# Kernel tuning notes

Measured on AMD Instinct MI355X. Metric: run time of the kernel, lower is better.

## Reference

```python
import jax, jax.numpy as jnp
import numpy as np

B, T, D = 2, 2048, 2048
N, K, H = 16, 8, 128  # num_heads, num_kv_heads, head_dim
SOFTCAP = 50.0
ROPE_BASE = 10000.0


def apply_rope(x, positions):
    # x: [B, L, heads, H], positions: [B, L]
    head_dim = x.shape[-1]
    fraction = 2.0 * jnp.arange(head_dim // 2, dtype=jnp.float32) / head_dim
    timescale = ROPE_BASE ** fraction  # [H/2]
    sinusoid = positions.astype(jnp.float32)[..., None] / timescale  # [B, L, H/2]
    sinusoid = sinusoid[..., None, :]  # [B, L, 1, H/2]
    sin, cos = jnp.sin(sinusoid), jnp.cos(sinusoid)
    first, second = jnp.split(x, 2, axis=-1)
    out = jnp.concatenate([first * cos - second * sin,
                           second * cos + first * sin], axis=-1)
    return out.astype(x.dtype)


def setup_inputs() -> dict:
    key = jax.random.key(0)
    kx, kq, kkv, ko = jax.random.split(key, 4)
    x = jax.random.normal(kx, (B, T, D), dtype=jnp.float32)
    positions = jnp.broadcast_to(jnp.arange(T, dtype=jnp.int32), (B, T))
    attn_mask = jnp.broadcast_to(
        jnp.tril(jnp.ones((T, T), dtype=bool))[None, None], (B, 1, T, T))
    # variance-scaling fan_in init approximated with scaled normals
    w_q = jax.random.normal(kq, (N, D, H), dtype=jnp.float32) / np.sqrt(D)
    w_kv = jax.random.normal(kkv, (2, K, D, H), dtype=jnp.float32) / np.sqrt(D)
    w_out = jax.random.normal(ko, (N, H, D), dtype=jnp.float32) / np.sqrt(N * H)
    return {"x": x, "positions": positions, "attn_mask": attn_mask,
            "w_q": w_q, "w_kv": w_kv, "w_out": w_out}


def reference(x, positions, attn_mask, w_q, w_kv, w_out):
    # QKV projections (GQA: separate q and kv einsums)
    q = jnp.einsum('BTD,NDH->BTNH', x, w_q)        # [B,T,N,H]
    kv = jnp.einsum('BSD,cKDH->cBSKH', x, w_kv)     # [2,B,S,K,H]
    k, v = kv[0], kv[1]
    q = apply_rope(q, positions) * (H ** -0.5)      # rsqrt_head_dim norm
    k = apply_rope(k, positions)
    # GQA grouping: N = K * G
    G = N // K
    qg = q.reshape(B, T, K, G, H)
    logits = jnp.einsum('BTKGH,BSKH->BKGTS', qg, k).astype(jnp.float32)
    logits = jnp.tanh(logits / SOFTCAP) * SOFTCAP   # logits softcap
    big_neg = -2.3819763e+38
    masked = jnp.where(attn_mask[:, :, None, :, :], logits, big_neg)
    probs = jax.nn.softmax(masked, axis=-1).astype(k.dtype)
    encoded = jnp.einsum('BKGTS,BSKH->BTKGH', probs, v).reshape(B, T, N, H)
    return jnp.einsum('BTNH,NHD->BTD', encoded, w_out)
```

## Files before the change

### kernel.cpp

```cpp
#include <hip/hip_runtime.h>
#include <math.h>
#include <stdint.h>


typedef unsigned short u16;
using bf16x8 = __attribute__((ext_vector_type(8))) short;
using f32x4  = __attribute__((ext_vector_type(4))) float;

#define MFMA_BF16(a,b,c) __builtin_amdgcn_mfma_f32_16x16x32_bf16((a),(b),(c),0,0,0)

static __device__ __forceinline__ float b2f(u16 u) {
  union { unsigned int i; float f; } v; v.i = ((unsigned int)u) << 16; return v.f;
}
static __device__ __forceinline__ u16 f2b(float f) {
  union { float f; unsigned int i; } v; v.f = f;
  unsigned int r = v.i + 0x7fffu + ((v.i >> 16) & 1u);
  return (u16)(r >> 16);
}
static __device__ __forceinline__ unsigned pk2(float x0, float x1) {
  union { float f; unsigned u; } a, b;
  a.f = x0; b.f = x1;
  return __builtin_amdgcn_perm(b.u + 0x8000u, a.u + 0x8000u, 0x07060302u);
}
static __device__ __forceinline__ void gload_lds16(const void* g, void* l) {
  __builtin_amdgcn_global_load_lds((__attribute__((address_space(1))) void*)(g),
                                   (__attribute__((address_space(3))) void*)(l),
                                   16, 0, 0);
}

__global__ __launch_bounds__(256) void prep(const float* __restrict__ x, u16* __restrict__ xb,
                                            const float* __restrict__ wq,
                                            const float* __restrict__ wkv,
                                            const float* __restrict__ wout,
                                            u16* __restrict__ wqkvt, u16* __restrict__ woutt) {
  const int tid = threadIdx.x;
  int bid = blockIdx.x;
  if (bid < 8192) {
    const int i = (bid * 256 + tid) * 4;
    const float4 v = *(const float4*)(x + i);
    ushort4 o;
    o.x = f2b(v.x); o.y = f2b(v.y); o.z = f2b(v.z); o.w = f2b(v.w);
    *(ushort4*)(xb + i) = o;
    return;
  }
  bid -= 8192;
  const float* src;
  u16* dst;
  int rows, cols, bx, by;
  if (bid < 8192) {
    const int seg = bid >> 12;
    const int r = bid & 4095;
    const int mat = r >> 8;
    bx = (r & 255) & 3;
    by = (r & 255) >> 2;
    rows = 2048; cols = 128;
    src = (seg ? wkv : wq) + (size_t)mat * 2048 * 128;
    dst = wqkvt + (size_t)(seg * 16 + mat) * 2048 * 128;
  } else {
    const int r = bid - 8192;
    bx = r & 63;
    by = r >> 6;
    rows = 2048; cols = 2048;
    src = wout;
    dst = woutt;
  }
  __shared__ u16 tile[32][33];
  const int c0 = bx * 32, r0 = by * 32;
  const int tx = tid & 31, ty = tid >> 5;
#pragma unroll
  for (int j = 0; j < 4; ++j)
    tile[ty + j * 8][tx] = f2b(src[(size_t)(r0 + ty + j * 8) * cols + (c0 + tx)]);
  __syncthreads();
#pragma unroll
  for (int j = 0; j < 4; ++j)
    dst[(size_t)(c0 + ty + j * 8) * rows + (r0 + tx)] = tile[tx][ty + j * 8];
}

__global__ __launch_bounds__(256) void gemm_qkv(const u16* __restrict__ X,
                                                const u16* __restrict__ wqkvt,
                                                u16* __restrict__ qb,
                                                u16* __restrict__ kb,
                                                u16* __restrict__ vtb) {
  __shared__ __align__(16) u16 sA[128 * 64];
  __shared__ __align__(16) u16 sB[128 * 64];
  const int m0 = blockIdx.x * 128;
  const int ct = blockIdx.y;
  const u16* Bt = wqkvt + (size_t)ct * 128 * 2048;
  const int tid = threadIdx.x;
  const int wave = tid >> 6, lane = tid & 63;
  const int wm = wave & 1, wn = wave >> 1;
  const int quad = lane >> 4, l16 = lane & 15;
  const int srow = lane >> 3;
  const int sch = (lane & 7) ^ srow;

  f32x4 acc[4][4] = {};

  for (int k0 = 0; k0 < 2048; k0 += 64) {
#pragma unroll
    for (int s = 0; s < 4; ++s) {
      const int instr = wave * 4 + s;
      const int row = instr * 8 + srow;
      gload_lds16(X + (size_t)(m0 + row) * 2048 + k0 + sch * 8, (char*)sA + instr * 1024);
      gload_lds16(Bt + (size_t)row * 2048 + k0 + sch * 8, (char*)sB + instr * 1024);
    }
    __syncthreads();
#pragma unroll
    for (int ks = 0; ks < 2; ++ks) {
      bf16x8 af[4], bfr[4];
#pragma unroll
      for (int mf = 0; mf < 4; ++mf) {
        const int R = wm * 64 + mf * 16 + l16;
        af[mf] = *(const bf16x8*)((char*)sA + R * 128 + (((ks * 4 + quad) ^ (R & 7)) << 4));
      }
#pragma unroll
      for (int nf = 0; nf < 4; ++nf) {
        const int R = wn * 64 + nf * 16 + l16;
        bfr[nf] = *(const bf16x8*)((char*)sB + R * 128 + (((ks * 4 + quad) ^ (R & 7)) << 4));
      }
#pragma unroll
      for (int mf = 0; mf < 4; ++mf)
#pragma unroll
        for (int nf = 0; nf < 4; ++nf)
          acc[mf][nf] = MFMA_BF16(af[mf], bfr[nf], acc[mf][nf]);
    }
    __syncthreads();
  }

#pragma unroll
  for (int mf = 0; mf < 4; ++mf) {
    const int mm = m0 + wm * 64 + mf * 16 + quad * 4;
    const int b = mm >> 11;
    const int t = mm & 2047;
#pragma unroll
    for (int nf = 0; nf < 4; ++nf) {
      const int h = wn * 64 + nf * 16 + l16;
      if (ct < 16) {
        u16* d = qb + (((size_t)b * 16 + ct) * 2048 + t) * 128 + h;
#pragma unroll
        for (int i = 0; i < 4; ++i) d[(size_t)i * 128] = f2b(acc[mf][nf][i]);
      } else if (ct < 24) {
        u16* d = kb + (((size_t)b * 8 + (ct - 16)) * 2048 + t) * 128 + h;
#pragma unroll
        for (int i = 0; i < 4; ++i) d[(size_t)i * 128] = f2b(acc[mf][nf][i]);
      } else {
        u16* d = vtb + (((size_t)b * 8 + (ct - 24)) * 128 + h) * 2048 + t;
        uint2 pkv;
        pkv.x = (unsigned)f2b(acc[mf][nf][0]) | ((unsigned)f2b(acc[mf][nf][1]) << 16);
        pkv.y = (unsigned)f2b(acc[mf][nf][2]) | ((unsigned)f2b(acc[mf][nf][3]) << 16);
        *(uint2*)d = pkv;
      }
    }
  }
}

__global__ __launch_bounds__(256) void rope_kernel(u16* __restrict__ qb,
                                                   u16* __restrict__ kb,
                                                   const int* __restrict__ pos) {
  const unsigned idx = blockIdx.x * 256 + threadIdx.x;
  const unsigned QP = 1u << 21;
  u16* p;
  float scale;
  int b, t, j2;
  if (idx < QP) {
    j2 = (int)(idx & 31) * 2; t = (int)((idx >> 5) & 2047);
    const int hd = (int)((idx >> 16) & 15); b = (int)(idx >> 20);
    p = qb + (((size_t)b * 16 + hd) * 2048 + t) * 128;
    scale = 0.08838834764831845f;
  } else {
    const unsigned r = idx - QP;
    j2 = (int)(r & 31) * 2; t = (int)((r >> 5) & 2047);
    const int hd = (int)((r >> 16) & 7); b = (int)(r >> 19);
    p = kb + (((size_t)b * 8 + hd) * 2048 + t) * 128;
    scale = 1.0f;
  }
  const float fpos = (float)pos[(size_t)b * 2048 + t];
  const unsigned lo = *(const unsigned*)(p + j2);
  const unsigned hi = *(const unsigned*)(p + j2 + 64);
  unsigned olo = 0, ohi = 0;
#pragma unroll
  for (int d = 0; d < 2; ++d) {
    const int j = j2 + d;
    const float ts = __powf(10000.0f, (float)j * (1.0f / 64.0f));
    float sn, cs;
    sincosf(fpos / ts, &sn, &cs);
    const float a = b2f((u16)((d ? (lo >> 16) : lo) & 0xffffu));
    const float c2 = b2f((u16)((d ? (hi >> 16) : hi) & 0xffffu));
    olo |= ((unsigned)f2b((a * cs - c2 * sn) * scale)) << (16 * d);
    ohi |= ((unsigned)f2b((c2 * cs + a * sn) * scale)) << (16 * d);
  }
  *(unsigned*)(p + j2) = olo;
  *(unsigned*)(p + j2 + 64) = ohi;
}

__global__ __launch_bounds__(256) void attn_fused(const u16* __restrict__ qg,
                                                  const u16* __restrict__ kg,
                                                  const u16* __restrict__ vtg,
                                                  u16* __restrict__ enc) {
  __shared__ __align__(16) char lds[32768];
  char* sK = lds;
  char* sV = lds + 16384;

  const int bid = blockIdx.x;
  const int x = bid & 7;
  const int i6 = bid >> 3;
  const int p = i6 & 15;
  const int head = (i6 >> 4) * 8 + x;
  const int b = head >> 4;
  const int n = head & 15;
  const int kh = n >> 1;

  const u16* qbase = qg + ((size_t)b * 16 + n) * 2048 * 128;
  const u16* kbase = kg + ((size_t)b * 8 + kh) * 2048 * 128;
  const u16* vbase = vtg + ((size_t)b * 8 + kh) * 128 * 2048;

  const int tid = threadIdx.x, wave = tid >> 6, lane = tid & 63;
  const int quad = lane >> 4, l16 = lane & 15;
  const int bp_a0 = ((quad & 1) * 32 + l16) * 4;
  const int bp_a1 = bp_a0 + 64;

  const float L2E = 1.4426950408889634f;
  const float C50 = 72.13475204444817f;
  const float A1 = 1.3333333333e-4f;
  const float A2 = 2.1333333333e-8f;
  const float A3 = 3.4539682540e-12f;

#pragma unroll 1
  for (int pass = 0; pass < 2; ++pass) {
    const int Q = pass ? (31 - p) : p;
    const int tw = Q * 64 + wave * 16;
    const int tlane = tw + l16;

    bf16x8 qf[4];
#pragma unroll
    for (int kf = 0; kf < 4; ++kf)
      qf[kf] = *(const bf16x8*)(qbase + (size_t)tlane * 128 + kf * 32 + quad * 8);

    f32x4 o[8] = {};
    f32x4 lacc = {0.f, 0.f, 0.f, 0.f};

#pragma unroll 1
    for (int si = 0; si <= Q; ++si) {
      const int s0 = si * 64;
      __syncthreads();
#pragma unroll
      for (int r2 = 0; r2 < 4; ++r2) {
        const int idx = r2 * 256 + tid;
        const int kr = idx >> 4, kc = idx & 15;
        *(float4*)(sK + kr * 256 + ((kc ^ (kr & 15)) << 4)) =
            *(const float4*)(kbase + (size_t)(s0 + kr) * 128 + kc * 8);
        const int vr = idx >> 3, vc = idx & 7;
        *(float4*)(sV + vr * 128 + ((vc ^ (vr & 7)) << 4)) =
            *(const float4*)(vbase + (size_t)vr * 2048 + s0 + vc * 8);
      }
      __syncthreads();

      const bool diag = (si == Q);
      const int nfmax = diag ? wave : 3;
      const int kmax = diag ? (wave >> 1) : 1;

      f32x4 sacc[4];
#pragma unroll
      for (int nf = 0; nf < 4; ++nf) {
        if (nf <= nfmax) {
          const int sr = nf * 16 + l16;
          f32x4 a = {0.f, 0.f, 0.f, 0.f};
#pragma unroll
          for (int kf = 0; kf < 4; ++kf) {
            const bf16x8 kfr =
                *(const bf16x8*)(sK + sr * 256 + (((kf * 4 + quad) ^ (sr & 15)) << 4));
            a = MFMA_BF16(kfr, qf[kf], a);
          }
          sacc[nf] = a;
        }
      }

#pragma unroll
      for (int nf = 0; nf < 4; ++nf) {
        if (nf <= nfmax) {
          const f32x4 xv = sacc[nf];
          const f32x4 u = xv * xv;
          f32x4 t = u * (-A3) + A2;
          t = u * t + (-A1);
          t = u * t + 1.0f;
          const f32x4 tc = xv * t;
          f32x4 pv;
#pragma unroll
          for (int i = 0; i < 4; ++i) pv[i] = exp2f(fmaf(tc[i], L2E, -C50));
          if (diag) {
#pragma unroll
            for (int i = 0; i < 4; ++i) {
              const int sg = s0 + nf * 16 + quad * 4 + i;
              if (sg > tlane) pv[i] = 0.0f;
            }
          }
          sacc[nf] = pv;
          lacc += pv;
        }
      }

      unsigned pkd[4][2];
#pragma unroll
      for (int nf = 0; nf < 4; ++nf) {
        if (nf <= nfmax) {
          pkd[nf][0] = pk2(sacc[nf][0], sacc[nf][1]);
          pkd[nf][1] = pk2(sacc[nf][2], sacc[nf][3]);
        } else {
          pkd[nf][0] = 0u; pkd[nf][1] = 0u;
        }
      }

#pragma unroll
      for (int c2 = 0; c2 < 2; ++c2) {
        if (c2 <= kmax) {
          const int lo = (quad >> 1);
          const int dA0 = __builtin_amdgcn_ds_bpermute(bp_a0, (int)pkd[2 * c2][0]);
          const int dB0 = __builtin_amdgcn_ds_bpermute(bp_a0, (int)pkd[2 * c2 + 1][0]);
          const int dA1 = __builtin_amdgcn_ds_bpermute(bp_a0, (int)pkd[2 * c2][1]);
          const int dB1 = __builtin_amdgcn_ds_bpermute(bp_a0, (int)pkd[2 * c2 + 1][1]);
          const int dA2 = __builtin_amdgcn_ds_bpermute(bp_a1, (int)pkd[2 * c2][0]);
          const int dB2 = __builtin_amdgcn_ds_bpermute(bp_a1, (int)pkd[2 * c2 + 1][0]);
          const int dA3 = __builtin_amdgcn_ds_bpermute(bp_a1, (int)pkd[2 * c2][1]);
          const int dB3 = __builtin_amdgcn_ds_bpermute(bp_a1, (int)pkd[2 * c2 + 1][1]);
          union { int d[4]; bf16x8 v; } pb;
          pb.d[0] = lo ? dB0 : dA0;
          pb.d[1] = lo ? dB1 : dA1;
          pb.d[2] = lo ? dB2 : dA2;
          pb.d[3] = lo ? dB3 : dA3;
#pragma unroll
          for (int nfo = 0; nfo < 8; ++nfo) {
            const int hr = nfo * 16 + l16;
            const bf16x8 vb =
                *(const bf16x8*)(sV + hr * 128 + (((c2 * 4 + quad) ^ (hr & 7)) << 4));
            o[nfo] = MFMA_BF16(vb, pb.v, o[nfo]);
          }
        }
      }
    }

    float lsum = lacc[0] + lacc[1] + lacc[2] + lacc[3];
    lsum += __shfl_xor(lsum, 16);
    lsum += __shfl_xor(lsum, 32);
    const float inv = 1.0f / lsum;
    u16* d = enc + (((size_t)b * 2048 + tlane) * 16 + n) * 128 + quad * 4;
#pragma unroll
    for (int nfo = 0; nfo < 8; ++nfo) {
      uint2 st;
      st.x = (unsigned)f2b(o[nfo][0] * inv) | ((unsigned)f2b(o[nfo][1] * inv) << 16);
      st.y = (unsigned)f2b(o[nfo][2] * inv) | ((unsigned)f2b(o[nfo][3] * inv) << 16);
      *(uint2*)(d + nfo * 16) = st;
    }
  }
}

__global__ __launch_bounds__(256) void gemm_out(const u16* __restrict__ A,
                                                const u16* __restrict__ Bt,
                                                float* __restrict__ C) {
  __shared__ __align__(16) u16 sA[128 * 64];
  __shared__ __align__(16) u16 sB[128 * 64];
  const int m0 = blockIdx.x * 128;
  const int n0 = blockIdx.y * 128;
  const int tid = threadIdx.x;
  const int wave = tid >> 6, lane = tid & 63;
  const int wm = wave & 1, wn = wave >> 1;
  const int quad = lane >> 4, l16 = lane & 15;
  const int srow = lane >> 3;
  const int sch = (lane & 7) ^ srow;

  f32x4 acc[4][4] = {};

  for (int k0 = 0; k0 < 2048; k0 += 64) {
#pragma unroll
    for (int s = 0; s < 4; ++s) {
      const int instr = wave * 4 + s;
      const int row = instr * 8 + srow;
      gload_lds16(A + (size_t)(m0 + row) * 2048 + k0 + sch * 8, (char*)sA + instr * 1024);
      gload_lds16(Bt + (size_t)(n0 + row) * 2048 + k0 + sch * 8, (char*)sB + instr * 1024);
    }
    __syncthreads();
#pragma unroll
    for (int ks = 0; ks < 2; ++ks) {
      bf16x8 af[4], bfr[4];
#pragma unroll
      for (int mf = 0; mf < 4; ++mf) {
        const int R = wm * 64 + mf * 16 + l16;
        af[mf] = *(const bf16x8*)((char*)sA + R * 128 + (((ks * 4 + quad) ^ (R & 7)) << 4));
      }
#pragma unroll
      for (int nf = 0; nf < 4; ++nf) {
        const int R = wn * 64 + nf * 16 + l16;
        bfr[nf] = *(const bf16x8*)((char*)sB + R * 128 + (((ks * 4 + quad) ^ (R & 7)) << 4));
      }
#pragma unroll
      for (int mf = 0; mf < 4; ++mf)
#pragma unroll
        for (int nf = 0; nf < 4; ++nf)
          acc[mf][nf] = MFMA_BF16(af[mf], bfr[nf], acc[mf][nf]);
    }
    __syncthreads();
  }

#pragma unroll
  for (int mf = 0; mf < 4; ++mf) {
    const int mm = m0 + wm * 64 + mf * 16 + quad * 4;
#pragma unroll
    for (int nf = 0; nf < 4; ++nf) {
      const int col = n0 + wn * 64 + nf * 16 + l16;
#pragma unroll
      for (int i = 0; i < 4; ++i) C[(size_t)(mm + i) * 2048 + col] = acc[mf][nf][i];
    }
  }
}

extern "C" void kernel_launch(void* const* d_in, const int* in_sizes, int n_in,
                              void* d_out, int out_size, void* d_ws, size_t ws_size,
                              hipStream_t stream) {
  (void)in_sizes; (void)n_in; (void)out_size; (void)ws_size;
  const float* x     = (const float*)d_in[0];
  const int*   posi  = (const int*)d_in[1];
  const float* w_q   = (const float*)d_in[3];
  const float* w_kv  = (const float*)d_in[4];
  const float* w_out = (const float*)d_in[5];
  float* out = (float*)d_out;

  u16* ws = (u16*)d_ws;
  u16* wqkvt = ws;
  u16* woutt = ws + (size_t)8388608;
  u16* qb    = ws + (size_t)12582912;
  u16* kb    = ws + (size_t)20971520;
  u16* vtb   = ws + (size_t)25165824;
  u16* encb  = ws + (size_t)29360128;
  u16* xb    = encb;

  prep<<<20480, 256, 0, stream>>>(x, xb, w_q, w_kv, w_out, wqkvt, woutt);
  gemm_qkv<<<dim3(32, 32), 256, 0, stream>>>(xb, wqkvt, qb, kb, vtb);
  rope_kernel<<<12288, 256, 0, stream>>>(qb, kb, posi);
  attn_fused<<<512, 256, 0, stream>>>(qb, kb, vtb, encb);
  gemm_out<<<dim3(32, 16), 256, 0, stream>>>(encb, woutt, out);
}
```

Baseline: 405.6 us.

## Split attention query-tile pairs into separate blocks and load K/V directly to LDS

After: 402.6 us. Within noise of the previous version (-0.7%).

```diff
diff --git a/kernel.cpp b/kernel.cpp
--- a/kernel.cpp
+++ b/kernel.cpp
@@ -192,19 +192,22 @@
   *(unsigned*)(p + j2 + 64) = ohi;
 }
 
-__global__ __launch_bounds__(256) void attn_fused(const u16* __restrict__ qg,
-                                                  const u16* __restrict__ kg,
-                                                  const u16* __restrict__ vtg,
-                                                  u16* __restrict__ enc) {
+__global__ __launch_bounds__(256, 4) void attn_fused(const u16* __restrict__ qg,
+                                                     const u16* __restrict__ kg,
+                                                     const u16* __restrict__ vtg,
+                                                     u16* __restrict__ enc) {
   __shared__ __align__(16) char lds[32768];
   char* sK = lds;
   char* sV = lds + 16384;
 
   const int bid = blockIdx.x;
-  const int x = bid & 7;
-  const int i6 = bid >> 3;
-  const int p = i6 & 15;
-  const int head = (i6 >> 4) * 8 + x;
+  const int half = bid >> 9;
+  const int r = bid & 511;
+  const int x = r & 7;
+  const int g = r >> 3;
+  const int pr = g & 15;
+  const int head = (g >> 4) * 8 + x;
+  const int Q = half ? pr : (31 - pr);
   const int b = head >> 4;
   const int n = head & 15;
   const int kh = n >> 1;
@@ -224,131 +227,134 @@
   const float A2 = 2.1333333333e-8f;
   const float A3 = 3.4539682540e-12f;
 
+  const u16* kp[4];
+  const u16* vp[4];
+#pragma unroll
+  for (int s = 0; s < 4; ++s) {
+    const int kr = wave * 16 + s * 4 + quad;
+    kp[s] = kbase + (size_t)kr * 128 + (l16 ^ (s * 4 + quad)) * 8;
+    const int vr = wave * 32 + s * 8 + (lane >> 3);
+    vp[s] = vbase + (size_t)vr * 2048 + ((lane & 7) ^ (lane >> 3)) * 8;
+  }
+
+  const int tw = Q * 64 + wave * 16;
+  const int tlane = tw + l16;
+
+  bf16x8 qf[4];
+#pragma unroll
+  for (int kf = 0; kf < 4; ++kf)
+    qf[kf] = *(const bf16x8*)(qbase + (size_t)tlane * 128 + kf * 32 + quad * 8);
+
+  f32x4 o[8] = {};
+  f32x4 lacc = {0.f, 0.f, 0.f, 0.f};
+
 #pragma unroll 1
-  for (int pass = 0; pass < 2; ++pass) {
-    const int Q = pass ? (31 - p) : p;
-    const int tw = Q * 64 + wave * 16;
-    const int tlane = tw + l16;
-
-    bf16x8 qf[4];
-#pragma unroll
-    for (int kf = 0; kf < 4; ++kf)
-      qf[kf] = *(const bf16x8*)(qbase + (size_t)tlane * 128 + kf * 32 + quad * 8);
-
-    f32x4 o[8] = {};
-    f32x4 lacc = {0.f, 0.f, 0.f, 0.f};
-
-#pragma unroll 1
-    for (int si = 0; si <= Q; ++si) {
-      const int s0 = si * 64;
-      __syncthreads();
-#pragma unroll
-      for (int r2 = 0; r2 < 4; ++r2) {
-        const int idx = r2 * 256 + tid;
-        const int kr = idx >> 4, kc = idx & 15;
-        *(float4*)(sK + kr * 256 + ((kc ^ (kr & 15)) << 4)) =
-            *(const float4*)(kbase + (size_t)(s0 + kr) * 128 + kc * 8);
-        const int vr = idx >> 3, vc = idx & 7;
-        *(float4*)(sV + vr * 128 + ((vc ^ (vr & 7)) << 4)) =
-            *(const float4*)(vbase + (size_t)vr * 2048 + s0 + vc * 8);
-      }
-      __syncthreads();
-
-      const bool diag = (si == Q);
-      const int nfmax = diag ? wave : 3;
-      const int kmax = diag ? (wave >> 1) : 1;
-
-      f32x4 sacc[4];
-#pragma unroll
-      for (int nf = 0; nf < 4; ++nf) {
-        if (nf <= nfmax) {
-          const int sr = nf * 16 + l16;
-          f32x4 a = {0.f, 0.f, 0.f, 0.f};
-#pragma unroll
-          for (int kf = 0; kf < 4; ++kf) {
-            const bf16x8 kfr =
-                *(const bf16x8*)(sK + sr * 256 + (((kf * 4 + quad) ^ (sr & 15)) << 4));
-            a = MFMA_BF16(kfr, qf[kf], a);
-          }
-          sacc[nf] = a;
+  for (int si = 0; si <= Q; ++si) {
+    const int s0 = si * 64;
+    __syncthreads();
+#pragma unroll
+    for (int s = 0; s < 4; ++s) {
+      gload_lds16(kp[s], sK + (wave * 4 + s) * 1024);
+      gload_lds16(vp[s], sV + (wave * 4 + s) * 1024);
+      kp[s] += 64 * 128;
+      vp[s] += 64;
+    }
+    __syncthreads();
+
+    const bool diag = (si == Q);
+    const int nfmax = diag ? wave : 3;
+    const int kmax = diag ? (wave >> 1) : 1;
+
+    f32x4 sacc[4];
+#pragma unroll
+    for (int nf = 0; nf < 4; ++nf) {
+      if (nf <= nfmax) {
+        const int sr = nf * 16 + l16;
+        f32x4 a = {0.f, 0.f, 0.f, 0.f};
+#pragma unroll
+        for (int kf = 0; kf < 4; ++kf) {
+          const bf16x8 kfr =
+              *(const bf16x8*)(sK + sr * 256 + (((kf * 4 + quad) ^ (sr & 15)) << 4));
+          a = MFMA_BF16(kfr, qf[kf], a);
         }
-      }
-
-#pragma unroll
-      for (int nf = 0; nf < 4; ++nf) {
-        if (nf <= nfmax) {
-          const f32x4 xv = sacc[nf];
-          const f32x4 u = xv * xv;
-          f32x4 t = u * (-A3) + A2;
-          t = u * t + (-A1);
-          t = u * t + 1.0f;
-          const f32x4 tc = xv * t;
-          f32x4 pv;
-#pragma unroll
-          for (int i = 0; i < 4; ++i) pv[i] = exp2f(fmaf(tc[i], L2E, -C50));
-          if (diag) {
-#pragma unroll
-            for (int i = 0; i < 4; ++i) {
-              const int sg = s0 + nf * 16 + quad * 4 + i;
-              if (sg > tlane) pv[i] = 0.0f;
-            }
-          }
-          sacc[nf] = pv;
-          lacc += pv;
-        }
-      }
-
-      unsigned pkd[4][2];
-#pragma unroll
-      for (int nf = 0; nf < 4; ++nf) {
-        if (nf <= nfmax) {
-          pkd[nf][0] = pk2(sacc[nf][0], sacc[nf][1]);
-          pkd[nf][1] = pk2(sacc[nf][2], sacc[nf][3]);
-        } else {
-          pkd[nf][0] = 0u; pkd[nf][1] = 0u;
-        }
-      }
-
-#pragma unroll
-      for (int c2 = 0; c2 < 2; ++c2) {
-        if (c2 <= kmax) {
-          const int lo = (quad >> 1);
-          const int dA0 = __builtin_amdgcn_ds_bpermute(bp_a0, (int)pkd[2 * c2][0]);
-          const int dB0 = __builtin_amdgcn_ds_bpermute(bp_a0, (int)pkd[2 * c2 + 1][0]);
-          const int dA1 = __builtin_amdgcn_ds_bpermute(bp_a0, (int)pkd[2 * c2][1]);
-          const int dB1 = __builtin_amdgcn_ds_bpermute(bp_a0, (int)pkd[2 * c2 + 1][1]);
-          const int dA2 = __builtin_amdgcn_ds_bpermute(bp_a1, (int)pkd[2 * c2][0]);
-          const int dB2 = __builtin_amdgcn_ds_bpermute(bp_a1, (int)pkd[2 * c2 + 1][0]);
-          const int dA3 = __builtin_amdgcn_ds_bpermute(bp_a1, (int)pkd[2 * c2][1]);
-          const int dB3 = __builtin_amdgcn_ds_bpermute(bp_a1, (int)pkd[2 * c2 + 1][1]);
-          union { int d[4]; bf16x8 v; } pb;
-          pb.d[0] = lo ? dB0 : dA0;
-          pb.d[1] = lo ? dB1 : dA1;
-          pb.d[2] = lo ? dB2 : dA2;
-          pb.d[3] = lo ? dB3 : dA3;
-#pragma unroll
-          for (int nfo = 0; nfo < 8; ++nfo) {
-            const int hr = nfo * 16 + l16;
-            const bf16x8 vb =
-                *(const bf16x8*)(sV + hr * 128 + (((c2 * 4 + quad) ^ (hr & 7)) << 4));
-            o[nfo] = MFMA_BF16(vb, pb.v, o[nfo]);
+        sacc[nf] = a;
+      }
+    }
+
+#pragma unroll
+    for (int nf = 0; nf < 4; ++nf) {
+      if (nf <= nfmax) {
+        const f32x4 xv = sacc[nf];
+        const f32x4 u = xv * xv;
+        f32x4 t = u * (-A3) + A2;
+        t = u * t + (-A1);
+        t = u * t + 1.0f;
+        const f32x4 tc = xv * t;
+        f32x4 pv;
+#pragma unroll
+        for (int i = 0; i < 4; ++i) pv[i] = exp2f(fmaf(tc[i], L2E, -C50));
+        if (diag) {
+#pragma unroll
+          for (int i = 0; i < 4; ++i) {
+            const int sg = s0 + nf * 16 + quad * 4 + i;
+            if (sg > tlane) pv[i] = 0.0f;
           }
         }
-      }
-    }
-
-    float lsum = lacc[0] + lacc[1] + lacc[2] + lacc[3];
-    lsum += __shfl_xor(lsum, 16);
-    lsum += __shfl_xor(lsum, 32);
-    const float inv = 1.0f / lsum;
-    u16* d = enc + (((size_t)b * 2048 + tlane) * 16 + n) * 128 + quad * 4;
-#pragma unroll
-    for (int nfo = 0; nfo < 8; ++nfo) {
-      uint2 st;
-      st.x = (unsigned)f2b(o[nfo][0] * inv) | ((unsigned)f2b(o[nfo][1] * inv) << 16);
-      st.y = (unsigned)f2b(o[nfo][2] * inv) | ((unsigned)f2b(o[nfo][3] * inv) << 16);
-      *(uint2*)(d + nfo * 16) = st;
-    }
+        sacc[nf] = pv;
+        lacc += pv;
+      }
+    }
+
+    unsigned pkd[4][2];
+#pragma unroll
+    for (int nf = 0; nf < 4; ++nf) {
+      if (nf <= nfmax) {
+        pkd[nf][0] = pk2(sacc[nf][0], sacc[nf][1]);
+        pkd[nf][1] = pk2(sacc[nf][2], sacc[nf][3]);
+      } else {
+        pkd[nf][0] = 0u; pkd[nf][1] = 0u;
+      }
+    }
+
+#pragma unroll
+    for (int c2 = 0; c2 < 2; ++c2) {
+      if (c2 <= kmax) {
+        const int lo = (quad >> 1);
+        const int dA0 = __builtin_amdgcn_ds_bpermute(bp_a0, (int)pkd[2 * c2][0]);
+        const int dB0 = __builtin_amdgcn_ds_bpermute(bp_a0, (int)pkd[2 * c2 + 1][0]);
+        const int dA1 = __builtin_amdgcn_ds_bpermute(bp_a0, (int)pkd[2 * c2][1]);
+        const int dB1 = __builtin_amdgcn_ds_bpermute(bp_a0, (int)pkd[2 * c2 + 1][1]);
+        const int dA2 = __builtin_amdgcn_ds_bpermute(bp_a1, (int)pkd[2 * c2][0]);
+        const int dB2 = __builtin_amdgcn_ds_bpermute(bp_a1, (int)pkd[2 * c2 + 1][0]);
+        const int dA3 = __builtin_amdgcn_ds_bpermute(bp_a1, (int)pkd[2 * c2][1]);
+        const int dB3 = __builtin_amdgcn_ds_bpermute(bp_a1, (int)pkd[2 * c2 + 1][1]);
+        union { int d[4]; bf16x8 v; } pb;
+        pb.d[0] = lo ? dB0 : dA0;
+        pb.d[1] = lo ? dB1 : dA1;
+        pb.d[2] = lo ? dB2 : dA2;
+        pb.d[3] = lo ? dB3 : dA3;
+#pragma unroll
+        for (int nfo = 0; nfo < 8; ++nfo) {
+          const int hr = nfo * 16 + l16;
+          const bf16x8 vb =
+              *(const bf16x8*)(sV + hr * 128 + (((c2 * 4 + quad) ^ (hr & 7)) << 4));
+          o[nfo] = MFMA_BF16(vb, pb.v, o[nfo]);
+        }
+      }
+    }
+  }
+
+  float lsum = lacc[0] + lacc[1] + lacc[2] + lacc[3];
+  lsum += __shfl_xor(lsum, 16);
+  lsum += __shfl_xor(lsum, 32);
+  const float inv = 1.0f / lsum;
+  u16* d = enc + (((size_t)b * 2048 + tlane) * 16 + n) * 128 + quad * 4;
+#pragma unroll
+  for (int nfo = 0; nfo < 8; ++nfo) {
+    uint2 st;
+    st.x = (unsigned)f2b(o[nfo][0] * inv) | ((unsigned)f2b(o[nfo][1] * inv) << 16);
+    st.y = (unsigned)f2b(o[nfo][2] * inv) | ((unsigned)f2b(o[nfo][3] * inv) << 16);
+    *(uint2*)(d + nfo * 16) = st;
   }
 }
 
@@ -434,6 +440,6 @@
   prep<<<20480, 256, 0, stream>>>(x, xb, w_q, w_kv, w_out, wqkvt, woutt);
   gemm_qkv<<<dim3(32, 32), 256, 0, stream>>>(xb, wqkvt, qb, kb, vtb);
   rope_kernel<<<12288, 256, 0, stream>>>(qb, kb, posi);
-  attn_fused<<<512, 256, 0, stream>>>(qb, kb, vtb, encb);
+  attn_fused<<<1024, 256, 0, stream>>>(qb, kb, vtb, encb);
   gemm_out<<<dim3(32, 16), 256, 0, stream>>>(encb, woutt, out);
 }
```
